# Kernel tuning notes

Measured on AMD Instinct MI355X. Metric: run time of the kernel, lower is better.

The kernel has to match this reference:

```python
import jax, jax.numpy as jnp
import numpy as np
from jax import lax

D_MODEL, D_INNER, D_STATE, DT_RANK, D_CONV = 512, 1024, 16, 32, 4
B, L = 4, 1024

def setup_inputs() -> dict:
    key = jax.random.key(0)
    ks = jax.random.split(key, 10)
    s = lambda k, shp, sc=0.02: jax.random.normal(k, shp, jnp.float32) * sc
    x = jax.random.normal(ks[0], (B, L, D_MODEL), jnp.float32)
    in_proj_w = s(ks[1], (2 * D_INNER, D_MODEL))
    conv_w = s(ks[2], (D_INNER, 1, D_CONV), 0.1)
    conv_b = jnp.zeros((D_INNER,), jnp.float32)
    x_proj_w = s(ks[3], (DT_RANK + 2 * D_STATE, D_INNER))
    dt_proj_w = s(ks[4], (D_INNER, DT_RANK), DT_RANK ** -0.5)
    dt_proj_b = s(ks[5], (D_INNER,), 0.1)
    # S4D-real init: A_log = log(1..d_state) per channel
    A_log = jnp.log(jnp.tile(jnp.arange(1, D_STATE + 1, dtype=jnp.float32), (D_INNER, 1)))
    D = jnp.ones((D_INNER,), jnp.float32)
    out_proj_w = s(ks[6], (D_MODEL, D_INNER))
    return dict(x=x, in_proj_w=in_proj_w, conv_w=conv_w, conv_b=conv_b,
                x_proj_w=x_proj_w, dt_proj_w=dt_proj_w, dt_proj_b=dt_proj_b,
                A_log=A_log, D=D, out_proj_w=out_proj_w)

def _mamba_fwd(x, in_proj_w, conv_w, conv_b, x_proj_w, dt_proj_w, dt_proj_b, A_log, D, out_proj_w):
    # in_proj and split into ssm branch / gate branch
    xz = jnp.einsum('bld,ed->ble', x, in_proj_w)          # [B,L,2*d_inner]
    xc, z = jnp.split(xz, 2, axis=-1)
    # depthwise causal conv1d along L (torch pads d_conv-1 both sides then slices [:L])
    xt = jnp.transpose(xc, (0, 2, 1))                      # [B,d_inner,L]
    xt = lax.conv_general_dilated(xt, conv_w, (1,), [(D_CONV - 1, 0)],
                                  feature_group_count=D_INNER,
                                  dimension_numbers=('NCH', 'OIH', 'NCH'))
    xc = jnp.transpose(xt + conv_b[None, :, None], (0, 2, 1))  # [B,L,d_inner]
    xc = jax.nn.silu(xc)
    # input-dependent SSM params
    dbc = jnp.einsum('bld,ed->ble', xc, x_proj_w)          # [B,L,dt_rank+2*d_state]
    dt, Bm, Cm = jnp.split(dbc, [DT_RANK, DT_RANK + D_STATE], axis=-1)
    delta = jax.nn.softplus(jnp.einsum('blr,dr->bld', dt, dt_proj_w) + dt_proj_b)  # [B,L,d_inner]
    A = -jnp.exp(A_log)                                    # [d_inner,d_state]
    deltaA = jnp.exp(delta[..., None] * A)                 # [B,L,d_inner,d_state]
    deltaBx = delta[..., None] * Bm[:, :, None, :] * xc[..., None]
    # parallel (associative) scan: h_t = deltaA_t * h_{t-1} + deltaBx_t
    def combine(c1, c2):
        a1, b1 = c1
        a2, b2 = c2
        return a2 * a1, a2 * b1 + b2
    _, h = lax.associative_scan(combine, (deltaA, deltaBx), axis=1)
    y = jnp.sum(h * Cm[:, :, None, :], axis=-1) + D * xc   # [B,L,d_inner]
    y = y * jax.nn.silu(z)
    return jnp.einsum('bld,ed->ble', y, out_proj_w)        # [B,L,d_model]

def reference(x, in_proj_w, conv_w, conv_b, x_proj_w, dt_proj_w, dt_proj_b, A_log, D, out_proj_w):
    return _mamba_fwd(x, in_proj_w, conv_w, conv_b, x_proj_w, dt_proj_w, dt_proj_b, A_log, D, out_proj_w)
```

## Files before the change

### kernel.cpp

```cpp
#include <hip/hip_runtime.h>
#include <cstddef>
#include <cstdint>

#define DMODEL 512
#define DINNER 1024
#define DSTATE 16
#define DTRANK 32
#define DCONV  4
#define NB     4
#define NL     1024
#define NR     (NB * NL)
#define CH     32
#define NCHUNK (NL / CH)
#define LOG2E  1.4426950408889634f

typedef __attribute__((ext_vector_type(8))) short bf16x8;
typedef __attribute__((ext_vector_type(4))) float f32x4;

__device__ __forceinline__ unsigned short f2bf(float f) {
    unsigned u = __builtin_bit_cast(unsigned, f);
    unsigned r = u + 0x7FFFu + ((u >> 16) & 1u);
    return (unsigned short)(r >> 16);
}

__device__ __forceinline__ void gload_lds16(const unsigned short* g, unsigned short* lds) {
    __builtin_amdgcn_global_load_lds(
        (const __attribute__((address_space(1))) void*)g,
        (__attribute__((address_space(3))) void*)lds, 16, 0, 0);
}

__global__ __launch_bounds__(256) void cast_bf16_kernel(
    const float* __restrict__ in, unsigned short* __restrict__ out, int n4)
{
    const int i = blockIdx.x * 256 + threadIdx.x;
    if (i >= n4) return;
    float4 v = ((const float4*)in)[i];
    ushort4 o;
    o.x = f2bf(v.x); o.y = f2bf(v.y); o.z = f2bf(v.z); o.w = f2bf(v.w);
    ((ushort4*)out)[i] = o;
}

template<int BN>
__global__ __launch_bounds__(256) void gemm_bf16_kernel(
    const unsigned short* __restrict__ A, const unsigned short* __restrict__ Bw,
    float* __restrict__ C, int M, int N, int K)
{
    constexpr int BK = 64;
    constexpr int NFRAG = BN / 32;
    constexpr int BINSTR = BN / 32;
    __shared__ unsigned short As[128 * BK];
    __shared__ unsigned short Bs[BN * BK];

    const int tid  = threadIdx.x;
    const int lane = tid & 63;
    const int w    = tid >> 6;
    const int wm   = w >> 1, wn = w & 1;
    const int brow = blockIdx.y * 128;
    const int bcol = blockIdx.x * BN;

    const int srcslot = (lane & 7) ^ (lane >> 3);
    const unsigned short* ag[4];
    unsigned short* al[4];
#pragma unroll
    for (int i = 0; i < 4; ++i) {
        const int r = w * 32 + i * 8 + (lane >> 3);
        ag[i] = A + (size_t)(brow + r) * K + srcslot * 8;
        al[i] = As + (w * 256 + i * 64) * 8;
    }
    const unsigned short* bg[BINSTR];
    unsigned short* bl[BINSTR];
#pragma unroll
    for (int i = 0; i < BINSTR; ++i) {
        const int r = w * 8 * BINSTR + i * 8 + (lane >> 3);
        bg[i] = Bw + (size_t)(bcol + r) * K + srcslot * 8;
        bl[i] = Bs + (w * 64 * BINSTR + i * 64) * 8;
    }

    const int fr = lane & 15;
    const int fq = lane >> 4;
    f32x4 acc[4][NFRAG] = {};

    for (int k0 = 0; k0 < K; k0 += BK) {
#pragma unroll
        for (int i = 0; i < 4; ++i) gload_lds16(ag[i] + k0, al[i]);
#pragma unroll
        for (int i = 0; i < BINSTR; ++i) gload_lds16(bg[i] + k0, bl[i]);
        __syncthreads();
#pragma unroll
        for (int ks = 0; ks < 2; ++ks) {
            bf16x8 af[4], bfr[NFRAG];
#pragma unroll
            for (int m = 0; m < 4; ++m) {
                const int r = wm * 64 + m * 16 + fr;
                const int s = (ks * 4 + fq) ^ (r & 7);
                af[m] = *(const bf16x8*)(As + r * BK + s * 8);
            }
#pragma unroll
            for (int n = 0; n < NFRAG; ++n) {
                const int r = wn * (BN / 2) + n * 16 + fr;
                const int s = (ks * 4 + fq) ^ (r & 7);
                bfr[n] = *(const bf16x8*)(Bs + r * BK + s * 8);
            }
#pragma unroll
            for (int m = 0; m < 4; ++m)
#pragma unroll
                for (int n = 0; n < NFRAG; ++n)
                    acc[m][n] = __builtin_amdgcn_mfma_f32_16x16x32_bf16(
                        af[m], bfr[n], acc[m][n], 0, 0, 0);
        }
        __syncthreads();
    }

    const int row0 = brow + wm * 64;
    const int col0 = bcol + wn * (BN / 2);
#pragma unroll
    for (int m = 0; m < 4; ++m)
#pragma unroll
        for (int n = 0; n < NFRAG; ++n)
#pragma unroll
            for (int j = 0; j < 4; ++j)
                C[(size_t)(row0 + m * 16 + fq * 4 + j) * N + col0 + n * 16 + fr] = acc[m][n][j];
}

__global__ __launch_bounds__(256) void conv_silu_kernel(
    const float* __restrict__ xz, const float* __restrict__ conv_w,
    const float* __restrict__ conv_b, float* __restrict__ xc)
{
    const int idx = blockIdx.x * 256 + threadIdx.x;
    const int e = idx & (DINNER - 1);
    const int r = idx >> 10;
    const int l = r & (NL - 1);
    float acc = conv_b[e];
    const float w0 = conv_w[e * 4 + 0], w1 = conv_w[e * 4 + 1];
    const float w2 = conv_w[e * 4 + 2], w3 = conv_w[e * 4 + 3];
    if (l >= 3) acc += w0 * xz[(size_t)(r - 3) * (2 * DINNER) + e];
    if (l >= 2) acc += w1 * xz[(size_t)(r - 2) * (2 * DINNER) + e];
    if (l >= 1) acc += w2 * xz[(size_t)(r - 1) * (2 * DINNER) + e];
    acc += w3 * xz[(size_t)r * (2 * DINNER) + e];
    const float sig = __builtin_amdgcn_rcpf(1.f + __builtin_amdgcn_exp2f(-acc * LOG2E));
    xc[idx] = acc * sig;
}

#define XPR 8
__global__ __launch_bounds__(256) void xpd_kernel(
    const float* __restrict__ xc, const float* __restrict__ W,
    const float* __restrict__ dtw, const float* __restrict__ dtb,
    float* __restrict__ dbc, float* __restrict__ delta)
{
    __shared__ float xr[XPR * DINNER];
    __shared__ float psum[XPR * 256];
    __shared__ float dlds[XPR * DTRANK];
    const int t = threadIdx.x;
    const int r0 = blockIdx.x * XPR;

    const float4* xc4 = (const float4*)(xc + (size_t)r0 * DINNER);
    float4* xr4 = (float4*)xr;
    for (int i = t; i < XPR * DINNER / 4; i += 256) xr4[i] = xc4[i];
    __syncthreads();

    const int j = t & 63, part = t >> 6;
    float acc[XPR];
#pragma unroll
    for (int row = 0; row < XPR; ++row) acc[row] = 0.f;
    const float4* w4  = (const float4*)(W + (size_t)j * DINNER) + part * 64;
    const float4* xb4 = (const float4*)xr + part * 64;
    for (int i = 0; i < 64; ++i) {
        const float4 w = w4[i];
#pragma unroll
        for (int row = 0; row < XPR; ++row) {
            const float4 xv = xb4[row * 256 + i];
            acc[row] += w.x * xv.x + w.y * xv.y + w.z * xv.z + w.w * xv.w;
        }
    }
#pragma unroll
    for (int row = 0; row < XPR; ++row) psum[row * 256 + part * 64 + j] = acc[row];
    __syncthreads();

    for (int o = t; o < XPR * 64; o += 256) {
        const int row = o >> 6, jj = o & 63;
        const float d = psum[row * 256 + jj] + psum[row * 256 + 64 + jj]
                      + psum[row * 256 + 128 + jj] + psum[row * 256 + 192 + jj];
        dbc[(size_t)(r0 + row) * 64 + jj] = d;
        if (jj < DTRANK) dlds[row * DTRANK + jj] = d;
    }
    __syncthreads();

#pragma unroll
    for (int rep = 0; rep < 4; ++rep) {
        const int e = rep * 256 + t;
        float4 wv[8];
        const float4* dtw4 = (const float4*)(dtw + (size_t)e * DTRANK);
#pragma unroll
        for (int q = 0; q < 8; ++q) wv[q] = dtw4[q];
        const float bias = dtb[e];
#pragma unroll
        for (int row = 0; row < XPR; ++row) {
            const float4* dl4 = (const float4*)(dlds + row * DTRANK);
            float sum = bias;
#pragma unroll
            for (int q = 0; q < 8; ++q) {
                const float4 dv = dl4[q];
                const float4 w = wv[q];
                sum += dv.x * w.x + dv.y * w.y + dv.z * w.z + dv.w * w.w;
            }
            delta[(size_t)(r0 + row) * DINNER + e] =
                fmaxf(sum, 0.f) + log1pf(__expf(-fabsf(sum)));
        }
    }
}

__global__ __launch_bounds__(256) void scanA_kernel(
    const float* __restrict__ delta, const float* __restrict__ xc,
    const float* __restrict__ dbc, const float* __restrict__ A_log,
    float* __restrict__ chunkP, float* __restrict__ chunkS)
{
    const int tid = threadIdx.x;
    const int e = blockIdx.x * 256 + tid;
    const int b = blockIdx.y, ck = blockIdx.z;
    const int rbase = b * NL + ck * CH;

    float Aes2[DSTATE];
    const float4* al4 = (const float4*)(A_log + (size_t)e * DSTATE);
#pragma unroll
    for (int q = 0; q < 4; ++q) {
        const float4 a = al4[q];
        Aes2[q * 4 + 0] = -__expf(a.x) * LOG2E;
        Aes2[q * 4 + 1] = -__expf(a.y) * LOG2E;
        Aes2[q * 4 + 2] = -__expf(a.z) * LOG2E;
        Aes2[q * 4 + 3] = -__expf(a.w) * LOG2E;
    }

    float S[DSTATE];
#pragma unroll
    for (int s = 0; s < DSTATE; ++s) S[s] = 0.f;
    float cum = 0.f;
    const float* dp = delta + (size_t)rbase * DINNER + e;
    const float* xp = xc + (size_t)rbase * DINNER + e;
    for (int l = 0; l < CH; ++l) {
        const float dl = dp[(size_t)l * DINNER];
        const float xv = xp[(size_t)l * DINNER];
        const float* bu = dbc + (size_t)(rbase + l) * 64 + DTRANK;
        cum += dl;
        const float common = dl * xv;
#pragma unroll
        for (int s = 0; s < DSTATE; ++s) {
            const float dA = __builtin_amdgcn_exp2f(dl * Aes2[s]);
            S[s] = fmaf(dA, S[s], common * bu[s]);
        }
    }
    const size_t oi = (((size_t)b * NCHUNK + ck) * DINNER + e) * DSTATE;
    float4* Pp = (float4*)(chunkP + oi);
    float4* Sp = (float4*)(chunkS + oi);
#pragma unroll
    for (int q = 0; q < 4; ++q) {
        float4 pv, sv;
        pv.x = __builtin_amdgcn_exp2f(cum * Aes2[q * 4 + 0]);
        pv.y = __builtin_amdgcn_exp2f(cum * Aes2[q * 4 + 1]);
        pv.z = __builtin_amdgcn_exp2f(cum * Aes2[q * 4 + 2]);
        pv.w = __builtin_amdgcn_exp2f(cum * Aes2[q * 4 + 3]);
        sv.x = S[q * 4 + 0]; sv.y = S[q * 4 + 1];
        sv.z = S[q * 4 + 2]; sv.w = S[q * 4 + 3];
        Pp[q] = pv; Sp[q] = sv;
    }
}

__global__ __launch_bounds__(256) void scanB_kernel(
    const float* __restrict__ chunkP, float* __restrict__ chunkS)
{
    const int idx = blockIdx.x * 256 + threadIdx.x;
    const int b = idx >> 14;
    const int rem = idx & (DINNER * DSTATE - 1);
    const size_t base = (size_t)b * NCHUNK * (DINNER * DSTATE) + rem;
    float P[NCHUNK], S[NCHUNK];
#pragma unroll
    for (int c = 0; c < NCHUNK; ++c) {
        P[c] = chunkP[base + (size_t)c * (DINNER * DSTATE)];
        S[c] = chunkS[base + (size_t)c * (DINNER * DSTATE)];
    }
    float h = 0.f;
#pragma unroll
    for (int c = 0; c < NCHUNK; ++c) {
        chunkS[base + (size_t)c * (DINNER * DSTATE)] = h;
        h = fmaf(P[c], h, S[c]);
    }
}

__global__ __launch_bounds__(256) void scanC_kernel(
    const float* __restrict__ xz, const float* __restrict__ xc,
    const float* __restrict__ dbc, const float* __restrict__ A_log,
    const float* __restrict__ Dp, const float* __restrict__ hinit,
    const float* __restrict__ delta, unsigned short* __restrict__ yh)
{
    const int tid = threadIdx.x;
    const int e = blockIdx.x * 256 + tid;
    const int b = blockIdx.y, ck = blockIdx.z;
    const int rbase = b * NL + ck * CH;

    float Aes2[DSTATE];
    const float4* al4 = (const float4*)(A_log + (size_t)e * DSTATE);
#pragma unroll
    for (int q = 0; q < 4; ++q) {
        const float4 a = al4[q];
        Aes2[q * 4 + 0] = -__expf(a.x) * LOG2E;
        Aes2[q * 4 + 1] = -__expf(a.y) * LOG2E;
        Aes2[q * 4 + 2] = -__expf(a.z) * LOG2E;
        Aes2[q * 4 + 3] = -__expf(a.w) * LOG2E;
    }

    float h[DSTATE];
    const size_t oi = (((size_t)b * NCHUNK + ck) * DINNER + e) * DSTATE;
    const float4* h4 = (const float4*)(hinit + oi);
#pragma unroll
    for (int q = 0; q < 4; ++q) {
        const float4 v = h4[q];
        h[q * 4 + 0] = v.x; h[q * 4 + 1] = v.y; h[q * 4 + 2] = v.z; h[q * 4 + 3] = v.w;
    }
    const float Dv = Dp[e];

    const float* dp = delta + (size_t)rbase * DINNER + e;
    const float* xp = xc + (size_t)rbase * DINNER + e;
    const float* zp = xz + (size_t)rbase * (2 * DINNER) + DINNER + e;
    unsigned short* yp = yh + (size_t)rbase * DINNER + e;

    for (int l = 0; l < CH; ++l) {
        const float dl = dp[(size_t)l * DINNER];
        const float xv = xp[(size_t)l * DINNER];
        const float zv = zp[(size_t)l * 2 * DINNER];
        const float* bu = dbc + (size_t)(rbase + l) * 64 + DTRANK;
        const float common = dl * xv;
        float y = 0.f;
#pragma unroll
        for (int s = 0; s < DSTATE; ++s) {
            const float dA = __builtin_amdgcn_exp2f(dl * Aes2[s]);
            h[s] = fmaf(dA, h[s], common * bu[s]);
            y = fmaf(h[s], bu[DSTATE + s], y);
        }
        y = fmaf(Dv, xv, y);
        const float sig = __builtin_amdgcn_rcpf(1.f + __builtin_amdgcn_exp2f(-zv * LOG2E));
        yp[(size_t)l * DINNER] = f2bf(y * (zv * sig));
    }
}

extern "C" void kernel_launch(void* const* d_in, const int* in_sizes, int n_in,
                              void* d_out, int out_size, void* d_ws, size_t ws_size,
                              hipStream_t stream)
{
    const float* x          = (const float*)d_in[0];
    const float* in_proj_w  = (const float*)d_in[1];
    const float* conv_w     = (const float*)d_in[2];
    const float* conv_b     = (const float*)d_in[3];
    const float* x_proj_w   = (const float*)d_in[4];
    const float* dt_proj_w  = (const float*)d_in[5];
    const float* dt_proj_b  = (const float*)d_in[6];
    const float* A_log      = (const float*)d_in[7];
    const float* Dp         = (const float*)d_in[8];
    const float* out_proj_w = (const float*)d_in[9];
    float* out = (float*)d_out;

    float* ws  = (float*)d_ws;
    float* xz     = ws;
    float* xc     = xz + (size_t)NR * 2 * DINNER;
    float* dbc    = xc + (size_t)NR * DINNER;
    float* yb     = dbc + (size_t)NR * 64;
    float* chunkS = yb + (size_t)NR * DINNER;
    unsigned short* yh  = (unsigned short*)(chunkS + (size_t)NB * NCHUNK * DINNER * DSTATE);
    unsigned short* xh  = yh;
    unsigned short* wih = yh + (size_t)NR * DINNER;
    unsigned short* woh = wih + (size_t)2 * DINNER * DMODEL;
    float* chunkP = out;

    cast_bf16_kernel<<<(NR * DMODEL / 4 + 255) / 256, 256, 0, stream>>>(x, xh, NR * DMODEL / 4);
    cast_bf16_kernel<<<(2 * DINNER * DMODEL / 4 + 255) / 256, 256, 0, stream>>>(
        in_proj_w, wih, 2 * DINNER * DMODEL / 4);
    cast_bf16_kernel<<<(DMODEL * DINNER / 4 + 255) / 256, 256, 0, stream>>>(
        out_proj_w, woh, DMODEL * DINNER / 4);

    gemm_bf16_kernel<128><<<dim3(2 * DINNER / 128, NR / 128), 256, 0, stream>>>(
        xh, wih, xz, NR, 2 * DINNER, DMODEL);
    conv_silu_kernel<<<NR * DINNER / 256, 256, 0, stream>>>(xz, conv_w, conv_b, xc);
    xpd_kernel<<<NR / XPR, 256, 0, stream>>>(xc, x_proj_w, dt_proj_w, dt_proj_b, dbc, yb);
    scanA_kernel<<<dim3(DINNER / 256, NB, NCHUNK), 256, 0, stream>>>(
        yb, xc, dbc, A_log, chunkP, chunkS);
    scanB_kernel<<<NB * DINNER * DSTATE / 256, 256, 0, stream>>>(chunkP, chunkS);
    scanC_kernel<<<dim3(DINNER / 256, NB, NCHUNK), 256, 0, stream>>>(
        xz, xc, dbc, A_log, Dp, chunkS, yb, yh);
    gemm_bf16_kernel<64><<<dim3(DMODEL / 64, NR / 128), 256, 0, stream>>>(
        yh, woh, out, NR, DMODEL, DINNER);
}
```

Before: 152.8 us.

## Move x_proj onto bf16 MFMA GEMM and merge weight casts into one kernel

The fp32 scalar x_proj stage inside xpd_kernel is replaced by the existing bf16 MFMA GEMM. conv_silu now also writes a bf16 copy of xc for that GEMM, and the delta/softplus computation becomes its own kernel that handles 16 rows per block. The three cast launches plus a new x_proj_w cast are merged into one kernel. This trades fp32 precision in dbc (B, C and dt) for bf16 inputs. The new GEMM launches only 32 blocks (N=64), so it may underuse the GPU.

```diff
diff --git a/kernel.cpp b/kernel.cpp
--- a/kernel.cpp
+++ b/kernel.cpp
@@ -29,15 +29,23 @@
         (__attribute__((address_space(3))) void*)lds, 16, 0, 0);
 }
 
-__global__ __launch_bounds__(256) void cast_bf16_kernel(
-    const float* __restrict__ in, unsigned short* __restrict__ out, int n4)
-{
-    const int i = blockIdx.x * 256 + threadIdx.x;
-    if (i >= n4) return;
-    float4 v = ((const float4*)in)[i];
+__global__ __launch_bounds__(256) void cast_all_kernel(
+    const float* __restrict__ x, const float* __restrict__ w_in,
+    const float* __restrict__ w_out, const float* __restrict__ w_xp,
+    unsigned short* __restrict__ xh, unsigned short* __restrict__ wih,
+    unsigned short* __restrict__ woh, unsigned short* __restrict__ xpwh)
+{
+    int i = blockIdx.x * 256 + threadIdx.x;
+    const float* src; unsigned short* dst;
+    if (i < 524288)       { src = x;     dst = xh;   }
+    else if (i < 786432)  { src = w_in;  dst = wih;  i -= 524288; }
+    else if (i < 917504)  { src = w_out; dst = woh;  i -= 786432; }
+    else if (i < 933888)  { src = w_xp;  dst = xpwh; i -= 917504; }
+    else return;
+    float4 v = ((const float4*)src)[i];
     ushort4 o;
     o.x = f2bf(v.x); o.y = f2bf(v.y); o.z = f2bf(v.z); o.w = f2bf(v.w);
-    ((ushort4*)out)[i] = o;
+    ((ushort4*)dst)[i] = o;
 }
 
 template<int BN>
@@ -124,7 +132,8 @@
 
 __global__ __launch_bounds__(256) void conv_silu_kernel(
     const float* __restrict__ xz, const float* __restrict__ conv_w,
-    const float* __restrict__ conv_b, float* __restrict__ xc)
+    const float* __restrict__ conv_b, float* __restrict__ xc,
+    unsigned short* __restrict__ xch)
 {
     const int idx = blockIdx.x * 256 + threadIdx.x;
     const int e = idx & (DINNER - 1);
@@ -138,53 +147,24 @@
     if (l >= 1) acc += w2 * xz[(size_t)(r - 1) * (2 * DINNER) + e];
     acc += w3 * xz[(size_t)r * (2 * DINNER) + e];
     const float sig = __builtin_amdgcn_rcpf(1.f + __builtin_amdgcn_exp2f(-acc * LOG2E));
-    xc[idx] = acc * sig;
-}
-
-#define XPR 8
-__global__ __launch_bounds__(256) void xpd_kernel(
-    const float* __restrict__ xc, const float* __restrict__ W,
-    const float* __restrict__ dtw, const float* __restrict__ dtb,
-    float* __restrict__ dbc, float* __restrict__ delta)
-{
-    __shared__ float xr[XPR * DINNER];
-    __shared__ float psum[XPR * 256];
-    __shared__ float dlds[XPR * DTRANK];
+    const float v = acc * sig;
+    xc[idx] = v;
+    xch[idx] = f2bf(v);
+}
+
+#define DROWS 16
+__global__ __launch_bounds__(256) void delta_kernel(
+    const float* __restrict__ dbc, const float* __restrict__ dtw,
+    const float* __restrict__ dtb, float* __restrict__ delta)
+{
+    __shared__ float dlds[DROWS * DTRANK];
     const int t = threadIdx.x;
-    const int r0 = blockIdx.x * XPR;
-
-    const float4* xc4 = (const float4*)(xc + (size_t)r0 * DINNER);
-    float4* xr4 = (float4*)xr;
-    for (int i = t; i < XPR * DINNER / 4; i += 256) xr4[i] = xc4[i];
+    const int r0 = blockIdx.x * DROWS;
+    for (int i = t; i < DROWS * DTRANK; i += 256) {
+        const int row = i >> 5, jj = i & 31;
+        dlds[i] = dbc[(size_t)(r0 + row) * 64 + jj];
+    }
     __syncthreads();
-
-    const int j = t & 63, part = t >> 6;
-    float acc[XPR];
-#pragma unroll
-    for (int row = 0; row < XPR; ++row) acc[row] = 0.f;
-    const float4* w4  = (const float4*)(W + (size_t)j * DINNER) + part * 64;
-    const float4* xb4 = (const float4*)xr + part * 64;
-    for (int i = 0; i < 64; ++i) {
-        const float4 w = w4[i];
-#pragma unroll
-        for (int row = 0; row < XPR; ++row) {
-            const float4 xv = xb4[row * 256 + i];
-            acc[row] += w.x * xv.x + w.y * xv.y + w.z * xv.z + w.w * xv.w;
-        }
-    }
-#pragma unroll
-    for (int row = 0; row < XPR; ++row) psum[row * 256 + part * 64 + j] = acc[row];
-    __syncthreads();
-
-    for (int o = t; o < XPR * 64; o += 256) {
-        const int row = o >> 6, jj = o & 63;
-        const float d = psum[row * 256 + jj] + psum[row * 256 + 64 + jj]
-                      + psum[row * 256 + 128 + jj] + psum[row * 256 + 192 + jj];
-        dbc[(size_t)(r0 + row) * 64 + jj] = d;
-        if (jj < DTRANK) dlds[row * DTRANK + jj] = d;
-    }
-    __syncthreads();
-
 #pragma unroll
     for (int rep = 0; rep < 4; ++rep) {
         const int e = rep * 256 + t;
@@ -194,7 +174,7 @@
         for (int q = 0; q < 8; ++q) wv[q] = dtw4[q];
         const float bias = dtb[e];
 #pragma unroll
-        for (int row = 0; row < XPR; ++row) {
+        for (int row = 0; row < DROWS; ++row) {
             const float4* dl4 = (const float4*)(dlds + row * DTRANK);
             float sum = bias;
 #pragma unroll
@@ -363,22 +343,23 @@
     float* dbc    = xc + (size_t)NR * DINNER;
     float* yb     = dbc + (size_t)NR * 64;
     float* chunkS = yb + (size_t)NR * DINNER;
-    unsigned short* yh  = (unsigned short*)(chunkS + (size_t)NB * NCHUNK * DINNER * DSTATE);
-    unsigned short* xh  = yh;
-    unsigned short* wih = yh + (size_t)NR * DINNER;
+    unsigned short* xch = (unsigned short*)(chunkS + (size_t)NB * NCHUNK * DINNER * DSTATE);
+    unsigned short* yh  = xch;
+    unsigned short* xh  = xch;
+    unsigned short* wih = xch + (size_t)NR * DINNER;
     unsigned short* woh = wih + (size_t)2 * DINNER * DMODEL;
+    unsigned short* xpwh = woh + (size_t)DMODEL * DINNER;
     float* chunkP = out;
 
-    cast_bf16_kernel<<<(NR * DMODEL / 4 + 255) / 256, 256, 0, stream>>>(x, xh, NR * DMODEL / 4);
-    cast_bf16_kernel<<<(2 * DINNER * DMODEL / 4 + 255) / 256, 256, 0, stream>>>(
-        in_proj_w, wih, 2 * DINNER * DMODEL / 4);
-    cast_bf16_kernel<<<(DMODEL * DINNER / 4 + 255) / 256, 256, 0, stream>>>(
-        out_proj_w, woh, DMODEL * DINNER / 4);
+    cast_all_kernel<<<(933888 + 255) / 256, 256, 0, stream>>>(
+        x, in_proj_w, out_proj_w, x_proj_w, xh, wih, woh, xpwh);
 
     gemm_bf16_kernel<128><<<dim3(2 * DINNER / 128, NR / 128), 256, 0, stream>>>(
         xh, wih, xz, NR, 2 * DINNER, DMODEL);
-    conv_silu_kernel<<<NR * DINNER / 256, 256, 0, stream>>>(xz, conv_w, conv_b, xc);
-    xpd_kernel<<<NR / XPR, 256, 0, stream>>>(xc, x_proj_w, dt_proj_w, dt_proj_b, dbc, yb);
+    conv_silu_kernel<<<NR * DINNER / 256, 256, 0, stream>>>(xz, conv_w, conv_b, xc, xch);
+    gemm_bf16_kernel<64><<<dim3(1, NR / 128), 256, 0, stream>>>(
+        xch, xpwh, dbc, NR, 64, DINNER);
+    delta_kernel<<<NR / DROWS, 256, 0, stream>>>(dbc, dt_proj_w, dt_proj_b, yb);
     scanA_kernel<<<dim3(DINNER / 256, NB, NCHUNK), 256, 0, stream>>>(
         yb, xc, dbc, A_log, chunkP, chunkS);
     scanB_kernel<<<NB * DINNER * DSTATE / 256, 256, 0, stream>>>(chunkP, chunkS);
```

Result: slower. 157.4 us (+3.0%).
